# Optimization experiments

Hardware: AMD Instinct MI355X
Metric: run time of the kernel (lower is better)

Reference implementation:

```python
import jax, jax.numpy as jnp
import numpy as np

EPS = 1e-5


def instance_norm(x):
    # InstanceNorm2d(affine=False): normalize each (b, c) map over spatial dims
    mean = x.mean(axis=(2, 3), keepdims=True)
    var = ((x - mean) ** 2).mean(axis=(2, 3), keepdims=True)
    return (x - mean) / jnp.sqrt(var + EPS)


def adder_conv_transpose(x, w, stride, padding):
    """AdderNet transposed 'convolution': standard transposed-conv geometry
    (zero-dilate input by stride, pad by k-1-padding, slide flipped kernel),
    but with the multiply-accumulate replaced by negative L1 distance:
        out[b,co,h,w] = -sum_{ci,i,j} |x_patch[b,ci,h+i,w+j] - w_flip[co,ci,i,j]|
    x: (B, Cin, H, W); w: (Cin, Cout, k, k) as in nn.ConvTranspose2d.
    """
    Cin, Cout, k, _ = w.shape
    B, _, H, W = x.shape
    s = stride
    Hd, Wd = (H - 1) * s + 1, (W - 1) * s + 1
    xd = jnp.zeros((B, Cin, Hd, Wd), x.dtype).at[:, :, ::s, ::s].set(x)
    p = k - 1 - padding
    xp = jnp.pad(xd, ((0, 0), (0, 0), (p, p), (p, p)))
    wf = jnp.flip(w, axis=(2, 3)).transpose(1, 0, 2, 3)  # (Cout, Cin, k, k)
    Ho = Hd + 2 * p - k + 1
    Wo = Wd + 2 * p - k + 1
    out = jnp.zeros((B, Cout, Ho, Wo), x.dtype)
    # fixed k*k taps (<=16): accumulate -|patch - weight| summed over Cin
    for i in range(k):
        for j in range(k):
            patch = xp[:, :, i:i + Ho, j:j + Wo]  # (B, Cin, Ho, Wo)
            wij = wf[:, :, i, j][None, :, :, None, None]  # (1, Cout, Cin, 1, 1)
            out = out - jnp.abs(patch[:, None] - wij).sum(axis=2)
    return out


_CFG = [  # (Cin, Cout, k, stride, pad)
    (100, 128, 4, 2, 1),
    (128, 64, 4, 2, 1),
    (64, 32, 3, 2, 1),
    (32, 16, 4, 2, 1),
    (16, 1, 4, 2, 1),
]


def setup_inputs() -> dict:
    key = jax.random.key(0)
    ks = jax.random.split(key, 6)
    inp = {"x": jax.random.normal(ks[0], (512, 100, 1, 1), dtype=jnp.float32)}
    for li, (cin, cout, k, _, _) in enumerate(_CFG):
        inp[f"w{li + 1}"] = 0.1 * jax.random.normal(ks[li + 1], (cin, cout, k, k), dtype=jnp.float32)
    return inp


def reference(x, w1, w2, w3, w4, w5):
    h = x
    for w, (_, _, k, s, p) in zip((w1, w2, w3, w4, w5), _CFG):
        h = adder_conv_transpose(h, w, s, p)
        h = instance_norm(h)
        h = jax.nn.relu(h)
    # final activation is Tanh (last ReLU in loop replaced below)
    return jnp.tanh(instance_norm(adder_conv_transpose_final_fixup(h)))


# NOTE: structure above would double-apply the last layer; define reference cleanly instead.

def adder_conv_transpose_final_fixup(h):  # placeholder, unused
    return h


def reference(x, w1, w2, w3, w4, w5):  # noqa: F811 (clean final definition)
    ws = (w1, w2, w3, w4, w5)
    h = x
    for li, (w, (_, _, k, s, p)) in enumerate(zip(ws, _CFG)):
        h = instance_norm(adder_conv_transpose(h, w, s, p))
        h = jnp.tanh(h) if li == 4 else jax.nn.relu(h)
    return h  # (B, 1, 28, 28)
```

## Files before the change

### kernel.cpp

```cpp
#include <hip/hip_runtime.h>
#include <math.h>

#define NB 512

#define OFF_T1 0
#define OFF_T2 2048
#define OFF_T3 3072
#define OFF_T4 3360
#define OFF_T5 3616
#define OFF_WT1 4096
#define OFF_WT2 208896
#define OFF_WT3 339968
#define OFF_WT4 358400
#define OFF_WT5 366592
#define OFF_ACT 366848
#define OFF_Y   1972480

__device__ __forceinline__ void loadv(float (&d)[1], const float* p){ d[0]=*p; }
__device__ __forceinline__ void loadv(float (&d)[2], const float* p){ float2 v=*reinterpret_cast<const float2*>(p); d[0]=v.x; d[1]=v.y; }
__device__ __forceinline__ void loadv(float (&d)[4], const float* p){ float4 v=*reinterpret_cast<const float4*>(p); d[0]=v.x; d[1]=v.y; d[2]=v.z; d[3]=v.w; }
__device__ __forceinline__ void storev(float* p, const float (&d)[1]){ *p=d[0]; }
__device__ __forceinline__ void storev(float* p, const float (&d)[2]){ *reinterpret_cast<float2*>(p)=make_float2(d[0],d[1]); }
__device__ __forceinline__ void storev(float* p, const float (&d)[4]){ *reinterpret_cast<float4*>(p)=make_float4(d[0],d[1],d[2],d[3]); }

__global__ __launch_bounds__(256)
void prep1(const float* __restrict__ w1, const float* __restrict__ w2,
           const float* __restrict__ w3, const float* __restrict__ w4,
           const float* __restrict__ w5, const float* __restrict__ x,
           float* __restrict__ ws) {
  int idx = blockIdx.x * 256 + threadIdx.x;
  if (idx < 362752) {
    const float* W; int CIN, COUT, KK, e, wtb;
    if (idx < 204800)      { W=w1; CIN=100; COUT=128; KK=16; e=idx;        wtb=OFF_WT1; }
    else if (idx < 335872) { W=w2; CIN=128; COUT=64;  KK=16; e=idx-204800; wtb=OFF_WT2; }
    else if (idx < 354304) { W=w3; CIN=64;  COUT=32;  KK=9;  e=idx-335872; wtb=OFF_WT3; }
    else if (idx < 362496) { W=w4; CIN=32;  COUT=16;  KK=16; e=idx-354304; wtb=OFF_WT4; }
    else                   { W=w5; CIN=16;  COUT=1;   KK=16; e=idx-362496; wtb=OFF_WT5; }
    int ci = e / (COUT*KK); int rem = e % (COUT*KK); int co = rem / KK; int r = rem % KK;
    ws[wtb + (r*CIN + ci)*COUT + co] = W[e];
  } else {
    int j = idx - 362752;
    int b = j / 100, ci = j % 100;
    ws[OFF_ACT + ci*NB + b] = x[j];
  }
}

__global__ __launch_bounds__(256)
void prep2(float* __restrict__ ws) {
  int t = blockIdx.x * 256 + threadIdx.x;
  if (t >= 3632) return;
  int CIN, COUT, wtb, tb, local;
  if (t < 2048)      { CIN=100; COUT=128; wtb=OFF_WT1; tb=OFF_T1; local=t; }
  else if (t < 3072) { CIN=128; COUT=64;  wtb=OFF_WT2; tb=OFF_T2; local=t-2048; }
  else if (t < 3360) { CIN=64;  COUT=32;  wtb=OFF_WT3; tb=OFF_T3; local=t-3072; }
  else if (t < 3616) { CIN=32;  COUT=16;  wtb=OFF_WT4; tb=OFF_T4; local=t-3360; }
  else               { CIN=16;  COUT=1;   wtb=OFF_WT5; tb=OFF_T5; local=t-3616; }
  int r = local / COUT, co = local % COUT;
  const float* wp = ws + wtb + (r*CIN)*COUT + co;
  float s = 0.f;
  for (int ci = 0; ci < CIN; ++ci) s += fabsf(wp[ci*COUT]);
  ws[tb + local] = s;
}

template<int CIN,int COUT,int K,int PAD,int HI,int WI,int HO,int WO,int R_CO,int R_B,int CS>
__global__ __launch_bounds__(64)
void conv_kernel(const float* __restrict__ X, const float* __restrict__ W,
                 const float* __restrict__ T, float* __restrict__ Y) {
  constexpr int S = HO*WO, NCOG = COUT/R_CO, NBG = NB/(64*R_B), CINS = CIN/CS;
  const int wid = blockIdx.x;
  const int q   = wid % S;
  const int t1  = wid / S;
  const int cog = t1 % NCOG;
  const int t2  = t1 / NCOG;
  const int bg  = t2 % NBG;
  const int cs  = t2 / NBG;
  const int oh = q / WO, ow = q % WO;
  const int co0 = cog * R_CO;
  const int b0  = bg*(64*R_B) + (int)threadIdx.x * R_B;
  const int ci0 = cs * CINS;

  float acc[R_CO][R_B];
  #pragma unroll
  for (int rc = 0; rc < R_CO; ++rc)
    #pragma unroll
    for (int rb = 0; rb < R_B; ++rb) acc[rc][rb] = 0.f;

  if (cs == 0) {
    float init[R_CO];
    #pragma unroll
    for (int rc = 0; rc < R_CO; ++rc) init[rc] = 0.f;
    #pragma unroll
    for (int kh = 0; kh < K; ++kh) {
      #pragma unroll
      for (int kw = 0; kw < K; ++kw) {
        const int th = oh + PAD - kh, tw = ow + PAD - kw;
        const bool real = (th >= 0) && !(th & 1) && ((th >> 1) < HI)
                       && (tw >= 0) && !(tw & 1) && ((tw >> 1) < WI);
        if (!real) {
          const float* tp = T + (kh*K + kw)*COUT + co0;
          #pragma unroll
          for (int rc = 0; rc < R_CO; ++rc) init[rc] += tp[rc];
        }
      }
    }
    #pragma unroll
    for (int rc = 0; rc < R_CO; ++rc)
      #pragma unroll
      for (int rb = 0; rb < R_B; ++rb) acc[rc][rb] = init[rc];
  }

  #pragma unroll
  for (int kh = 0; kh < K; ++kh) {
    const int th = oh + PAD - kh;
    if (th < 0 || (th & 1)) continue;
    const int ih = th >> 1;
    if (ih >= HI) continue;
    #pragma unroll
    for (int kw = 0; kw < K; ++kw) {
      const int tw = ow + PAD - kw;
      if (tw < 0 || (tw & 1)) continue;
      const int iw = tw >> 1;
      if (iw >= WI) continue;
      const int r = kh*K + kw, p = ih*WI + iw;
      const float* xp = X + (p*CIN + ci0)*NB + b0;
      const float* wp = W + (r*CIN + ci0)*COUT + co0;
      #pragma unroll 4
      for (int ci = 0; ci < CINS; ++ci) {
        float xv[R_B];
        loadv(xv, xp + ci*NB);
        #pragma unroll
        for (int rc = 0; rc < R_CO; ++rc) {
          const float wv = wp[ci*COUT + rc];
          #pragma unroll
          for (int rb = 0; rb < R_B; ++rb)
            acc[rc][rb] += fabsf(xv[rb] - wv);
        }
      }
    }
  }

  float* yp = Y + ((cs*S + q)*COUT + co0)*NB + b0;
  #pragma unroll
  for (int rc = 0; rc < R_CO; ++rc) storev(yp + rc*NB, acc[rc]);
}

template<int COUT,int S,int CS>
__global__ __launch_bounds__(256)
void norm_kernel(const float* __restrict__ Y, float* __restrict__ A) {
  __shared__ float red[4][64];
  __shared__ float stat[2][64];
  const int co = blockIdx.x % COUT;
  const int bg = blockIdx.x / COUT;
  const int lane = threadIdx.x & 63;
  const int w = threadIdx.x >> 6;
  const int b = bg*64 + lane;
  const float* yb = Y + co*NB + b;

  float s = 0.f;
  for (int q = w; q < S; q += 4) {
    float v = 0.f;
    #pragma unroll
    for (int cs = 0; cs < CS; ++cs) v += yb[(cs*S + q)*COUT*NB];
    s += v;
  }
  red[w][lane] = s;
  __syncthreads();
  if (w == 0) stat[0][lane] = (red[0][lane]+red[1][lane]+red[2][lane]+red[3][lane]) * (1.f/S);
  __syncthreads();
  const float mu = stat[0][lane];

  float s2 = 0.f;
  for (int q = w; q < S; q += 4) {
    float v = 0.f;
    #pragma unroll
    for (int cs = 0; cs < CS; ++cs) v += yb[(cs*S + q)*COUT*NB];
    const float d = v - mu;
    s2 += d*d;
  }
  red[w][lane] = s2;
  __syncthreads();
  if (w == 0) stat[1][lane] = rsqrtf((red[0][lane]+red[1][lane]+red[2][lane]+red[3][lane]) * (1.f/S) + 1e-5f);
  __syncthreads();
  const float rs = stat[1][lane];

  for (int q = w; q < S; q += 4) {
    float v = 0.f;
    #pragma unroll
    for (int cs = 0; cs < CS; ++cs) v += yb[(cs*S + q)*COUT*NB];
    const float n = (mu - v) * rs;
    A[(q*COUT + co)*NB + b] = fmaxf(n, 0.f);
  }
}

__global__ __launch_bounds__(256)
void norm5_kernel(const float* __restrict__ Y, float* __restrict__ out) {
  const int w = threadIdx.x >> 6, lane = threadIdx.x & 63;
  const int b = blockIdx.x*4 + w;
  const float* yb = Y + b;

  float s = 0.f;
  for (int q = lane; q < 784; q += 64) s += yb[q*NB];
  #pragma unroll
  for (int off = 1; off < 64; off <<= 1) s += __shfl_xor(s, off, 64);
  const float mu = s * (1.f/784.f);

  float s2 = 0.f;
  for (int q = lane; q < 784; q += 64) { float d = yb[q*NB] - mu; s2 += d*d; }
  #pragma unroll
  for (int off = 1; off < 64; off <<= 1) s2 += __shfl_xor(s2, off, 64);
  const float rs = rsqrtf(s2*(1.f/784.f) + 1e-5f);

  for (int q = lane; q < 784; q += 64) {
    const float n = (mu - yb[q*NB]) * rs;
    const float ax = fabsf(n);
    const float e = __expf(-2.f*ax);
    const float t = (1.f - e) / (1.f + e);
    out[b*784 + q] = copysignf(t, n);
  }
}

extern "C" void kernel_launch(void* const* d_in, const int* in_sizes, int n_in,
                              void* d_out, int out_size, void* d_ws, size_t ws_size,
                              hipStream_t stream) {
  const float* x  = (const float*)d_in[0];
  const float* w1 = (const float*)d_in[1];
  const float* w2 = (const float*)d_in[2];
  const float* w3 = (const float*)d_in[3];
  const float* w4 = (const float*)d_in[4];
  const float* w5 = (const float*)d_in[5];
  float* ws  = (float*)d_ws;
  float* out = (float*)d_out;

  float* ACT = ws + OFF_ACT;
  float* Y   = ws + OFF_Y;

  prep1<<<1617, 256, 0, stream>>>(w1, w2, w3, w4, w5, x, ws);
  prep2<<<15, 256, 0, stream>>>(ws);

  conv_kernel<100,128,4,1,  1, 1,  2, 2, 4,2,1><<< 512,64,0,stream>>>(ACT, ws+OFF_WT1, ws+OFF_T1, Y);
  norm_kernel<128,  4,1><<<1024,256,0,stream>>>(Y, ACT);

  conv_kernel<128, 64,4,1,  2, 2,  4, 4, 4,2,2><<<2048,64,0,stream>>>(ACT, ws+OFF_WT2, ws+OFF_T2, Y);
  norm_kernel< 64, 16,2><<< 512,256,0,stream>>>(Y, ACT);

  conv_kernel< 64, 32,3,1,  4, 4,  7, 7, 4,2,2><<<3136,64,0,stream>>>(ACT, ws+OFF_WT3, ws+OFF_T3, Y);
  norm_kernel< 32, 49,2><<< 256,256,0,stream>>>(Y, ACT);

  conv_kernel< 32, 16,4,1,  7, 7, 14,14, 4,2,1><<<3136,64,0,stream>>>(ACT, ws+OFF_WT4, ws+OFF_T4, Y);
  norm_kernel< 16,196,1><<< 128,256,0,stream>>>(Y, ACT);

  conv_kernel< 16,  1,4,1, 14,14, 28,28, 1,4,1><<<1568,64,0,stream>>>(ACT, ws+OFF_WT5, ws+OFF_T5, Y);
  norm5_kernel<<<128,256,0,stream>>>(Y, out);
}
```

Baseline: 253.8 us.

## Fuse all layers into one persistent cooperative kernel with grid syncs

Replaces the twelve separate launches (two prep kernels, five conv and five norm kernels) with one persistent cooperative kernel of 512 blocks that steps through eleven stages separated by grid.sync. It also drops the Cin split in the conv stages and the shared-memory reduction in the norm stages, and computes the weight abs-sum tables directly from the raw weights inside the prep stage. The aim is to remove per-launch overhead and inter-kernel gaps. In exchange, the work per stage is capped at 2048 waves, norm stages run one wave per (channel, batch-group) task serially over space with less parallelism, and grid-wide barriers add their own cost.

```diff
diff --git a/kernel.cpp b/kernel.cpp
--- a/kernel.cpp
+++ b/kernel.cpp
@@ -1,7 +1,11 @@
 #include <hip/hip_runtime.h>
+#include <hip/hip_cooperative_groups.h>
 #include <math.h>
 
+namespace cg = cooperative_groups;
+
 #define NB 512
+#define NWAVE 2048
 
 #define OFF_T1 0
 #define OFF_T2 2048
@@ -23,69 +27,55 @@
 __device__ __forceinline__ void storev(float* p, const float (&d)[2]){ *reinterpret_cast<float2*>(p)=make_float2(d[0],d[1]); }
 __device__ __forceinline__ void storev(float* p, const float (&d)[4]){ *reinterpret_cast<float4*>(p)=make_float4(d[0],d[1],d[2],d[3]); }
 
-__global__ __launch_bounds__(256)
-void prep1(const float* __restrict__ w1, const float* __restrict__ w2,
-           const float* __restrict__ w3, const float* __restrict__ w4,
-           const float* __restrict__ w5, const float* __restrict__ x,
-           float* __restrict__ ws) {
-  int idx = blockIdx.x * 256 + threadIdx.x;
-  if (idx < 362752) {
-    const float* W; int CIN, COUT, KK, e, wtb;
-    if (idx < 204800)      { W=w1; CIN=100; COUT=128; KK=16; e=idx;        wtb=OFF_WT1; }
-    else if (idx < 335872) { W=w2; CIN=128; COUT=64;  KK=16; e=idx-204800; wtb=OFF_WT2; }
-    else if (idx < 354304) { W=w3; CIN=64;  COUT=32;  KK=9;  e=idx-335872; wtb=OFF_WT3; }
-    else if (idx < 362496) { W=w4; CIN=32;  COUT=16;  KK=16; e=idx-354304; wtb=OFF_WT4; }
-    else                   { W=w5; CIN=16;  COUT=1;   KK=16; e=idx-362496; wtb=OFF_WT5; }
-    int ci = e / (COUT*KK); int rem = e % (COUT*KK); int co = rem / KK; int r = rem % KK;
-    ws[wtb + (r*CIN + ci)*COUT + co] = W[e];
-  } else {
-    int j = idx - 362752;
-    int b = j / 100, ci = j % 100;
-    ws[OFF_ACT + ci*NB + b] = x[j];
-  }
-}
-
-__global__ __launch_bounds__(256)
-void prep2(float* __restrict__ ws) {
-  int t = blockIdx.x * 256 + threadIdx.x;
-  if (t >= 3632) return;
-  int CIN, COUT, wtb, tb, local;
-  if (t < 2048)      { CIN=100; COUT=128; wtb=OFF_WT1; tb=OFF_T1; local=t; }
-  else if (t < 3072) { CIN=128; COUT=64;  wtb=OFF_WT2; tb=OFF_T2; local=t-2048; }
-  else if (t < 3360) { CIN=64;  COUT=32;  wtb=OFF_WT3; tb=OFF_T3; local=t-3072; }
-  else if (t < 3616) { CIN=32;  COUT=16;  wtb=OFF_WT4; tb=OFF_T4; local=t-3360; }
-  else               { CIN=16;  COUT=1;   wtb=OFF_WT5; tb=OFF_T5; local=t-3616; }
-  int r = local / COUT, co = local % COUT;
-  const float* wp = ws + wtb + (r*CIN)*COUT + co;
-  float s = 0.f;
-  for (int ci = 0; ci < CIN; ++ci) s += fabsf(wp[ci*COUT]);
-  ws[tb + local] = s;
-}
-
-template<int CIN,int COUT,int K,int PAD,int HI,int WI,int HO,int WO,int R_CO,int R_B,int CS>
-__global__ __launch_bounds__(64)
-void conv_kernel(const float* __restrict__ X, const float* __restrict__ W,
-                 const float* __restrict__ T, float* __restrict__ Y) {
-  constexpr int S = HO*WO, NCOG = COUT/R_CO, NBG = NB/(64*R_B), CINS = CIN/CS;
-  const int wid = blockIdx.x;
-  const int q   = wid % S;
-  const int t1  = wid / S;
-  const int cog = t1 % NCOG;
-  const int t2  = t1 / NCOG;
-  const int bg  = t2 % NBG;
-  const int cs  = t2 / NBG;
-  const int oh = q / WO, ow = q % WO;
-  const int co0 = cog * R_CO;
-  const int b0  = bg*(64*R_B) + (int)threadIdx.x * R_B;
-  const int ci0 = cs * CINS;
-
-  float acc[R_CO][R_B];
-  #pragma unroll
-  for (int rc = 0; rc < R_CO; ++rc)
-    #pragma unroll
-    for (int rb = 0; rb < R_B; ++rb) acc[rc][rb] = 0.f;
-
-  if (cs == 0) {
+__device__ void prep_stage(const float* __restrict__ w1, const float* __restrict__ w2,
+                           const float* __restrict__ w3, const float* __restrict__ w4,
+                           const float* __restrict__ w5, const float* __restrict__ x,
+                           float* __restrict__ ws, int gtid) {
+  for (int idx = gtid; idx < 417584; idx += 131072) {
+    if (idx < 362752) {
+      const float* W; int CIN, COUT, KK, e, wtb;
+      if (idx < 204800)      { W=w1; CIN=100; COUT=128; KK=16; e=idx;        wtb=OFF_WT1; }
+      else if (idx < 335872) { W=w2; CIN=128; COUT=64;  KK=16; e=idx-204800; wtb=OFF_WT2; }
+      else if (idx < 354304) { W=w3; CIN=64;  COUT=32;  KK=9;  e=idx-335872; wtb=OFF_WT3; }
+      else if (idx < 362496) { W=w4; CIN=32;  COUT=16;  KK=16; e=idx-354304; wtb=OFF_WT4; }
+      else                   { W=w5; CIN=16;  COUT=1;   KK=16; e=idx-362496; wtb=OFF_WT5; }
+      int ci = e / (COUT*KK); int rem = e % (COUT*KK); int co = rem / KK; int r = rem % KK;
+      ws[wtb + (r*CIN + ci)*COUT + co] = W[e];
+    } else if (idx < 413952) {
+      int j = idx - 362752;
+      int b = j / 100, ci = j % 100;
+      ws[OFF_ACT + ci*NB + b] = x[j];
+    } else {
+      int t = idx - 413952;
+      const float* W; int CIN, COUT, KK, tb, local;
+      if (t < 2048)      { W=w1; CIN=100; COUT=128; KK=16; tb=OFF_T1; local=t; }
+      else if (t < 3072) { W=w2; CIN=128; COUT=64;  KK=16; tb=OFF_T2; local=t-2048; }
+      else if (t < 3360) { W=w3; CIN=64;  COUT=32;  KK=9;  tb=OFF_T3; local=t-3072; }
+      else if (t < 3616) { W=w4; CIN=32;  COUT=16;  KK=16; tb=OFF_T4; local=t-3360; }
+      else               { W=w5; CIN=16;  COUT=1;   KK=16; tb=OFF_T5; local=t-3616; }
+      int r = local / COUT, co = local % COUT;
+      float s = 0.f;
+      #pragma unroll 4
+      for (int ci = 0; ci < CIN; ++ci) s += fabsf(W[(ci*COUT + co)*KK + r]);
+      ws[tb + local] = s;
+    }
+  }
+}
+
+template<int CIN,int COUT,int K,int PAD,int HI,int WI,int HO,int WO,int R_CO,int R_B>
+__device__ void conv_stage(const float* __restrict__ X, const float* __restrict__ W,
+                           const float* __restrict__ T, float* __restrict__ Y,
+                           int gw, int lane) {
+  constexpr int S = HO*WO, NCOG = COUT/R_CO, NBG = NB/(64*R_B), NT = S*NCOG*NBG;
+  for (int task = gw; task < NT; task += NWAVE) {
+    const int q   = task % S;
+    const int t1  = task / S;
+    const int cog = t1 % NCOG;
+    const int bg  = t1 / NCOG;
+    const int oh = q / WO, ow = q % WO;
+    const int co0 = cog * R_CO;
+    const int b0  = bg*(64*R_B) + lane * R_B;
+
     float init[R_CO];
     #pragma unroll
     for (int rc = 0; rc < R_CO; ++rc) init[rc] = 0.f;
@@ -103,119 +93,125 @@
         }
       }
     }
+    float acc[R_CO][R_B];
     #pragma unroll
     for (int rc = 0; rc < R_CO; ++rc)
       #pragma unroll
       for (int rb = 0; rb < R_B; ++rb) acc[rc][rb] = init[rc];
-  }
-
-  #pragma unroll
-  for (int kh = 0; kh < K; ++kh) {
-    const int th = oh + PAD - kh;
-    if (th < 0 || (th & 1)) continue;
-    const int ih = th >> 1;
-    if (ih >= HI) continue;
-    #pragma unroll
-    for (int kw = 0; kw < K; ++kw) {
-      const int tw = ow + PAD - kw;
-      if (tw < 0 || (tw & 1)) continue;
-      const int iw = tw >> 1;
-      if (iw >= WI) continue;
-      const int r = kh*K + kw, p = ih*WI + iw;
-      const float* xp = X + (p*CIN + ci0)*NB + b0;
-      const float* wp = W + (r*CIN + ci0)*COUT + co0;
-      #pragma unroll 4
-      for (int ci = 0; ci < CINS; ++ci) {
-        float xv[R_B];
-        loadv(xv, xp + ci*NB);
-        #pragma unroll
-        for (int rc = 0; rc < R_CO; ++rc) {
-          const float wv = wp[ci*COUT + rc];
+
+    #pragma unroll
+    for (int kh = 0; kh < K; ++kh) {
+      const int th = oh + PAD - kh;
+      if (th < 0 || (th & 1)) continue;
+      const int ih = th >> 1;
+      if (ih >= HI) continue;
+      #pragma unroll
+      for (int kw = 0; kw < K; ++kw) {
+        const int tw = ow + PAD - kw;
+        if (tw < 0 || (tw & 1)) continue;
+        const int iw = tw >> 1;
+        if (iw >= WI) continue;
+        const int r = kh*K + kw, p = ih*WI + iw;
+        const float* xp = X + (p*CIN)*NB + b0;
+        const float* wp = W + (r*CIN)*COUT + co0;
+        #pragma unroll 4
+        for (int ci = 0; ci < CIN; ++ci) {
+          float xv[R_B];
+          loadv(xv, xp + ci*NB);
           #pragma unroll
-          for (int rb = 0; rb < R_B; ++rb)
-            acc[rc][rb] += fabsf(xv[rb] - wv);
+          for (int rc = 0; rc < R_CO; ++rc) {
+            const float wv = wp[ci*COUT + rc];
+            #pragma unroll
+            for (int rb = 0; rb < R_B; ++rb)
+              acc[rc][rb] += fabsf(xv[rb] - wv);
+          }
         }
       }
     }
-  }
-
-  float* yp = Y + ((cs*S + q)*COUT + co0)*NB + b0;
-  #pragma unroll
-  for (int rc = 0; rc < R_CO; ++rc) storev(yp + rc*NB, acc[rc]);
-}
-
-template<int COUT,int S,int CS>
-__global__ __launch_bounds__(256)
-void norm_kernel(const float* __restrict__ Y, float* __restrict__ A) {
-  __shared__ float red[4][64];
-  __shared__ float stat[2][64];
-  const int co = blockIdx.x % COUT;
-  const int bg = blockIdx.x / COUT;
+    float* yp = Y + (q*COUT + co0)*NB + b0;
+    #pragma unroll
+    for (int rc = 0; rc < R_CO; ++rc) storev(yp + rc*NB, acc[rc]);
+  }
+}
+
+template<int COUT,int S>
+__device__ void norm_stage(const float* __restrict__ Y, float* __restrict__ A,
+                           int gw, int lane) {
+  constexpr int NT = COUT * (NB/64);
+  for (int task = gw; task < NT; task += NWAVE) {
+    const int co = task % COUT;
+    const int bg = task / COUT;
+    const int b = bg*64 + lane;
+    const float* yb = Y + co*NB + b;
+    float s = 0.f;
+    #pragma unroll 4
+    for (int q = 0; q < S; ++q) s += yb[q*COUT*NB];
+    const float mu = s * (1.f/S);
+    float v = 0.f;
+    #pragma unroll 4
+    for (int q = 0; q < S; ++q) { const float d = yb[q*COUT*NB] - mu; v += d*d; }
+    const float rs = rsqrtf(v * (1.f/S) + 1e-5f);
+    #pragma unroll 4
+    for (int q = 0; q < S; ++q) {
+      const float n = (mu - yb[q*COUT*NB]) * rs;
+      A[(q*COUT + co)*NB + b] = fmaxf(n, 0.f);
+    }
+  }
+}
+
+__device__ void norm5_stage(const float* __restrict__ Y, float* __restrict__ out,
+                            int gw, int lane) {
+  for (int b = gw; b < NB; b += NWAVE) {
+    const float* yb = Y + b;
+    float s = 0.f;
+    for (int q = lane; q < 784; q += 64) s += yb[q*NB];
+    #pragma unroll
+    for (int off = 1; off < 64; off <<= 1) s += __shfl_xor(s, off, 64);
+    const float mu = s * (1.f/784.f);
+    float s2 = 0.f;
+    for (int q = lane; q < 784; q += 64) { float d = yb[q*NB] - mu; s2 += d*d; }
+    #pragma unroll
+    for (int off = 1; off < 64; off <<= 1) s2 += __shfl_xor(s2, off, 64);
+    const float rs = rsqrtf(s2*(1.f/784.f) + 1e-5f);
+    for (int q = lane; q < 784; q += 64) {
+      const float n = (mu - yb[q*NB]) * rs;
+      const float ax = fabsf(n);
+      const float e = __expf(-2.f*ax);
+      const float t = (1.f - e) / (1.f + e);
+      out[b*784 + q] = copysignf(t, n);
+    }
+  }
+}
+
+__global__ __launch_bounds__(256, 2)
+void fused(const float* __restrict__ x,
+           const float* __restrict__ w1, const float* __restrict__ w2,
+           const float* __restrict__ w3, const float* __restrict__ w4,
+           const float* __restrict__ w5,
+           float* __restrict__ ws, float* __restrict__ out,
+           int s_lo, int s_hi) {
+  const int gtid = blockIdx.x*256 + threadIdx.x;
+  const int gw   = blockIdx.x*4 + (threadIdx.x >> 6);
   const int lane = threadIdx.x & 63;
-  const int w = threadIdx.x >> 6;
-  const int b = bg*64 + lane;
-  const float* yb = Y + co*NB + b;
-
-  float s = 0.f;
-  for (int q = w; q < S; q += 4) {
-    float v = 0.f;
-    #pragma unroll
-    for (int cs = 0; cs < CS; ++cs) v += yb[(cs*S + q)*COUT*NB];
-    s += v;
-  }
-  red[w][lane] = s;
-  __syncthreads();
-  if (w == 0) stat[0][lane] = (red[0][lane]+red[1][lane]+red[2][lane]+red[3][lane]) * (1.f/S);
-  __syncthreads();
-  const float mu = stat[0][lane];
-
-  float s2 = 0.f;
-  for (int q = w; q < S; q += 4) {
-    float v = 0.f;
-    #pragma unroll
-    for (int cs = 0; cs < CS; ++cs) v += yb[(cs*S + q)*COUT*NB];
-    const float d = v - mu;
-    s2 += d*d;
-  }
-  red[w][lane] = s2;
-  __syncthreads();
-  if (w == 0) stat[1][lane] = rsqrtf((red[0][lane]+red[1][lane]+red[2][lane]+red[3][lane]) * (1.f/S) + 1e-5f);
-  __syncthreads();
-  const float rs = stat[1][lane];
-
-  for (int q = w; q < S; q += 4) {
-    float v = 0.f;
-    #pragma unroll
-    for (int cs = 0; cs < CS; ++cs) v += yb[(cs*S + q)*COUT*NB];
-    const float n = (mu - v) * rs;
-    A[(q*COUT + co)*NB + b] = fmaxf(n, 0.f);
-  }
-}
-
-__global__ __launch_bounds__(256)
-void norm5_kernel(const float* __restrict__ Y, float* __restrict__ out) {
-  const int w = threadIdx.x >> 6, lane = threadIdx.x & 63;
-  const int b = blockIdx.x*4 + w;
-  const float* yb = Y + b;
-
-  float s = 0.f;
-  for (int q = lane; q < 784; q += 64) s += yb[q*NB];
-  #pragma unroll
-  for (int off = 1; off < 64; off <<= 1) s += __shfl_xor(s, off, 64);
-  const float mu = s * (1.f/784.f);
-
-  float s2 = 0.f;
-  for (int q = lane; q < 784; q += 64) { float d = yb[q*NB] - mu; s2 += d*d; }
-  #pragma unroll
-  for (int off = 1; off < 64; off <<= 1) s2 += __shfl_xor(s2, off, 64);
-  const float rs = rsqrtf(s2*(1.f/784.f) + 1e-5f);
-
-  for (int q = lane; q < 784; q += 64) {
-    const float n = (mu - yb[q*NB]) * rs;
-    const float ax = fabsf(n);
-    const float e = __expf(-2.f*ax);
-    const float t = (1.f - e) / (1.f + e);
-    out[b*784 + q] = copysignf(t, n);
+  float* ACT = ws + OFF_ACT;
+  float* Y   = ws + OFF_Y;
+  cg::grid_group grid = cg::this_grid();
+
+  for (int st = s_lo; st <= s_hi; ++st) {
+    switch (st) {
+      case 0: prep_stage(w1,w2,w3,w4,w5,x,ws,gtid); break;
+      case 1: conv_stage<100,128,4,1,  1, 1, 2, 2, 4, 2>(ACT, ws+OFF_WT1, ws+OFF_T1, Y, gw, lane); break;
+      case 2: norm_stage<128,  4>(Y, ACT, gw, lane); break;
+      case 3: conv_stage<128, 64,4,1,  2, 2, 4, 4, 4, 2>(ACT, ws+OFF_WT2, ws+OFF_T2, Y, gw, lane); break;
+      case 4: norm_stage< 64, 16>(Y, ACT, gw, lane); break;
+      case 5: conv_stage< 64, 32,3,1,  4, 4, 7, 7, 4, 2>(ACT, ws+OFF_WT3, ws+OFF_T3, Y, gw, lane); break;
+      case 6: norm_stage< 32, 49>(Y, ACT, gw, lane); break;
+      case 7: conv_stage< 32, 16,4,1,  7, 7,14,14, 4, 2>(ACT, ws+OFF_WT4, ws+OFF_T4, Y, gw, lane); break;
+      case 8: norm_stage< 16,196>(Y, ACT, gw, lane); break;
+      case 9: conv_stage< 16,  1,4,1, 14,14,28,28, 1, 4>(ACT, ws+OFF_WT5, ws+OFF_T5, Y, gw, lane); break;
+      case 10: norm5_stage(Y, out, gw, lane); break;
+    }
+    if (st < s_hi) grid.sync();
   }
 }
 
@@ -231,24 +227,13 @@
   float* ws  = (float*)d_ws;
   float* out = (float*)d_out;
 
-  float* ACT = ws + OFF_ACT;
-  float* Y   = ws + OFF_Y;
-
-  prep1<<<1617, 256, 0, stream>>>(w1, w2, w3, w4, w5, x, ws);
-  prep2<<<15, 256, 0, stream>>>(ws);
-
-  conv_kernel<100,128,4,1,  1, 1,  2, 2, 4,2,1><<< 512,64,0,stream>>>(ACT, ws+OFF_WT1, ws+OFF_T1, Y);
-  norm_kernel<128,  4,1><<<1024,256,0,stream>>>(Y, ACT);
-
-  conv_kernel<128, 64,4,1,  2, 2,  4, 4, 4,2,2><<<2048,64,0,stream>>>(ACT, ws+OFF_WT2, ws+OFF_T2, Y);
-  norm_kernel< 64, 16,2><<< 512,256,0,stream>>>(Y, ACT);
-
-  conv_kernel< 64, 32,3,1,  4, 4,  7, 7, 4,2,2><<<3136,64,0,stream>>>(ACT, ws+OFF_WT3, ws+OFF_T3, Y);
-  norm_kernel< 32, 49,2><<< 256,256,0,stream>>>(Y, ACT);
-
-  conv_kernel< 32, 16,4,1,  7, 7, 14,14, 4,2,1><<<3136,64,0,stream>>>(ACT, ws+OFF_WT4, ws+OFF_T4, Y);
-  norm_kernel< 16,196,1><<< 128,256,0,stream>>>(Y, ACT);
-
-  conv_kernel< 16,  1,4,1, 14,14, 28,28, 1,4,1><<<1568,64,0,stream>>>(ACT, ws+OFF_WT5, ws+OFF_T5, Y);
-  norm5_kernel<<<128,256,0,stream>>>(Y, out);
-}
+  int s_lo = 0, s_hi = 10;
+  void* args[] = {(void*)&x, (void*)&w1, (void*)&w2, (void*)&w3, (void*)&w4,
+                  (void*)&w5, (void*)&ws, (void*)&out, (void*)&s_lo, (void*)&s_hi};
+  hipError_t e = hipLaunchCooperativeKernel((const void*)fused, dim3(512), dim3(256),
+                                            args, 0, stream);
+  if (e != hipSuccess) {
+    for (int st = 0; st <= 10; ++st)
+      fused<<<512, 256, 0, stream>>>(x, w1, w2, w3, w4, w5, ws, out, st, st);
+  }
+}
```

After: 849.7 us. 3.35x slower.
